# Performance work log

Hardware: AMD Instinct MI355X
Metric: run time of the kernel (lower is better)

The kernel has to match this reference:

```python
import jax, jax.numpy as jnp
import numpy as np

B, N, D_IN, D_HEAD, H, D_EXPAND, D_OUT, D_TIME = 8, 1024, 512, 64, 8, 2048, 512, 256
DQ = D_HEAD * H          # 512
DV = D_IN * H            # 4096
D_QKV = 2 * DQ + 2 * DQ + DV
EPS = 1e-5

def _ln(x, g, b):
    m = jnp.mean(x, axis=-1, keepdims=True)
    v = jnp.var(x, axis=-1, keepdims=True)
    return (x - m) * jax.lax.rsqrt(v + EPS) * g + b

def _swish(x):
    return x * jax.nn.sigmoid(x)

def setup_inputs() -> dict:
    key = jax.random.key(0)
    ks = jax.random.split(key, 16)
    def lin(k, fan_in, fan_out):
        lim = 1.0 / np.sqrt(fan_in)
        kw, kb = jax.random.split(k)
        W = jax.random.uniform(kw, (fan_in, fan_out), jnp.float32, -lim, lim)
        b = jax.random.uniform(kb, (fan_out,), jnp.float32, -lim, lim)
        return W, b
    x = jax.random.normal(ks[0], (B, N, D_IN), jnp.float32)
    t = jax.random.normal(ks[1], (B, D_TIME), jnp.float32)
    Wqkv, bqkv = lin(ks[2], D_IN, D_QKV)
    Wm, bm = lin(ks[3], D_IN * H, D_IN)
    Wt1, bt1 = lin(ks[4], D_TIME, D_TIME)
    Wt2, bt2 = lin(ks[5], D_TIME, D_IN)
    Wf1, bf1 = lin(ks[6], D_IN, D_EXPAND)
    Wf2, bf2 = lin(ks[7], D_EXPAND, D_OUT)
    return {
        "x": x, "t": t,
        "ln1_g": jnp.ones((D_IN,)), "ln1_b": jnp.zeros((D_IN,)),
        "Wqkv": Wqkv, "bqkv": bqkv,
        "lam": jnp.float32(0.5),
        "Wm": Wm, "bm": bm,
        "Wt1": Wt1, "bt1": bt1, "Wt2": Wt2, "bt2": bt2,
        "lnf_g": jnp.ones((D_IN,)), "lnf_b": jnp.zeros((D_IN,)),
        "Wf1": Wf1, "bf1": bf1, "Wf2": Wf2, "bf2": bf2,
    }

def reference(x, t, ln1_g, ln1_b, Wqkv, bqkv, lam, Wm, bm,
              Wt1, bt1, Wt2, bt2, lnf_g, lnf_b, Wf1, bf1, Wf2, bf2):
    scale = D_HEAD ** (-0.5)
    qkv = _ln(x, ln1_g, ln1_b) @ Wqkv + bqkv            # [B,N,D_QKV]
    q1, q2, k1, k2, v = jnp.split(qkv, [DQ, 2 * DQ, 3 * DQ, 4 * DQ], axis=-1)
    hsplit = lambda a, c: a.reshape(B, N, H, c)          # [B,N,H,C]
    q1, q2 = hsplit(q1, D_HEAD), hsplit(q2, D_HEAD)
    k1, k2 = hsplit(k1, D_HEAD), hsplit(k2, D_HEAD)
    v = hsplit(v, D_IN)
    s1 = jax.nn.softmax(jnp.einsum('bnhc,bmhc->bhnm', q1, k1) * scale, axis=-1)
    s2 = jax.nn.softmax(jnp.einsum('bnhc,bmhc->bhnm', q2, k2) * scale, axis=-1)
    attn = s1 - lam * s2                                 # differential attention
    out = jnp.einsum('bhnm,bmhc->bnhc', attn, v).reshape(B, N, H * D_IN)
    x2 = x + out @ Wm + bm
    tp = (_swish(t @ Wt1 + bt1) @ Wt2 + bt2)[:, None, :]  # [B,1,d_in]
    h = _ln(x2 + tp, lnf_g, lnf_b)
    ff = _swish(h @ Wf1 + bf1) @ Wf2 + bf2
    return x2 + ff  # shortcut is identity (d_in == d_out)
```

## Files before the change

kernel.cpp:

```cpp
#include <hip/hip_runtime.h>

#define B_    8
#define N_    1024
#define DIN   512
#define H_    8
#define DH    64
#define DQKV  6144
#define DEXP  2048
#define DTIME 256

typedef __attribute__((ext_vector_type(8))) short s16x8;
typedef __attribute__((ext_vector_type(4))) short s16x4;
typedef __attribute__((ext_vector_type(4))) float f32x4;

__device__ __forceinline__ unsigned short f2bf(float f) {
  unsigned int u = __float_as_uint(f);
  u = (u + 0x7fffu + ((u >> 16) & 1u)) >> 16;
  return (unsigned short)u;
}

__device__ __forceinline__ void gload_lds16(const unsigned short* g, unsigned short* l) {
  __builtin_amdgcn_global_load_lds(
      (const __attribute__((address_space(1))) unsigned int*)(g),
      (__attribute__((address_space(3))) unsigned int*)(l), 16, 0, 0);
}

#define WAITV(n) do { asm volatile("s_waitcnt vmcnt(" #n ")" ::: "memory"); \
                      __builtin_amdgcn_sched_barrier(0); } while (0)
#define WAITL0() do { asm volatile("s_waitcnt lgkmcnt(0)" ::: "memory"); \
                      __builtin_amdgcn_sched_barrier(0); } while (0)

__global__ __launch_bounds__(256) void ln_k(
    const float* __restrict__ x, const float* __restrict__ add,
    const float* __restrict__ g, const float* __restrict__ bb,
    unsigned short* __restrict__ out)
{
  int row = blockIdx.x;
  int tid = threadIdx.x;
  const float* xr = x + (size_t)row * DIN;
  float v0 = xr[tid], v1 = xr[tid + 256];
  if (add) {
    const float* ar = add + (size_t)(row >> 10) * DIN;
    v0 += ar[tid]; v1 += ar[tid + 256];
  }
  float s = v0 + v1, sq = v0 * v0 + v1 * v1;
  #pragma unroll
  for (int m = 1; m < 64; m <<= 1) { s += __shfl_xor(s, m, 64); sq += __shfl_xor(sq, m, 64); }
  __shared__ float red[8];
  int w = tid >> 6;
  if ((tid & 63) == 0) { red[w] = s; red[4 + w] = sq; }
  __syncthreads();
  s  = red[0] + red[1] + red[2] + red[3];
  sq = red[4] + red[5] + red[6] + red[7];
  float mean = s * (1.0f / DIN);
  float var  = sq * (1.0f / DIN) - mean * mean;
  float rs = rsqrtf(var + 1e-5f);
  unsigned short* orow = out + (size_t)row * DIN;
  orow[tid]       = f2bf((v0 - mean) * rs * g[tid]       + bb[tid]);
  orow[tid + 256] = f2bf((v1 - mean) * rs * g[tid + 256] + bb[tid + 256]);
}

__global__ __launch_bounds__(256) void wtrans_k(
    const float* __restrict__ in, unsigned short* __restrict__ out, int R, int C)
{
  __shared__ float tile[32][33];
  int tx = threadIdx.x & 31, ty = threadIdx.x >> 5;
  int c0 = blockIdx.x * 32, r0 = blockIdx.y * 32;
  #pragma unroll
  for (int k = 0; k < 4; ++k)
    tile[ty + k * 8][tx] = in[(size_t)(r0 + ty + k * 8) * C + c0 + tx];
  __syncthreads();
  #pragma unroll
  for (int k = 0; k < 4; ++k)
    out[(size_t)(c0 + ty + k * 8) * R + r0 + tx] = f2bf(tile[tx][ty + k * 8]);
}

__global__ __launch_bounds__(256) void time_k(
    const float* __restrict__ t, const float* __restrict__ Wt1, const float* __restrict__ bt1,
    const float* __restrict__ Wt2, const float* __restrict__ bt2, float* __restrict__ tp)
{
  int b = blockIdx.x, tid = threadIdx.x;
  __shared__ float tl[256], hl[256];
  tl[tid] = t[(size_t)b * 256 + tid];
  __syncthreads();
  float a = bt1[tid];
  for (int k = 0; k < 256; ++k) a += tl[k] * Wt1[(size_t)k * 256 + tid];
  hl[tid] = a / (1.0f + __expf(-a));
  __syncthreads();
  for (int j = tid; j < 512; j += 256) {
    float a2 = bt2[j];
    for (int k = 0; k < 256; ++k) a2 += hl[k] * Wt2[(size_t)k * 512 + j];
    tp[(size_t)b * 512 + j] = a2;
  }
}

template<int EPI>
__global__ __launch_bounds__(256) void gemm_bt(
    const unsigned short* __restrict__ A, int lda,
    const unsigned short* __restrict__ Bt,
    const float* __restrict__ bias, const float* __restrict__ res,
    void* __restrict__ C, int ldc, int N, int K,
    unsigned short* __restrict__ vtout)
{
  __shared__ __attribute__((aligned(16))) unsigned short As[2 * 8192];
  __shared__ __attribute__((aligned(16))) unsigned short Bs[2 * 8192];
  int tid = threadIdx.x;
  int m0 = blockIdx.y * 128, n0 = blockIdx.x * 128;
  int lane = tid & 63, wid = tid >> 6;
  int wr = wid >> 1, wc = wid & 1;
  int lr = lane & 15, lg = lane >> 4, lk = lg * 8;
  f32x4 zero = {0.f, 0.f, 0.f, 0.f};
  f32x4 acc[4][4];
  #pragma unroll
  for (int i = 0; i < 4; ++i)
    #pragma unroll
    for (int j = 0; j < 4; ++j) acc[i][j] = zero;
  int srow = wid * 8 + (lane >> 3);
  int scol = ((lane & 7) ^ (lane >> 3)) * 8;
  const unsigned short* gA = A  + (size_t)(m0 + srow) * lda + scol;
  const unsigned short* gB = Bt + (size_t)(n0 + srow) * K + scol;
  int nk = K >> 6;
  #pragma unroll
  for (int i = 0; i < 4; ++i) {
    gload_lds16(gA + (size_t)(i * 32) * lda, As + (i * 32 + wid * 8) * 64);
    gload_lds16(gB + (size_t)(i * 32) * K,   Bs + (i * 32 + wid * 8) * 64);
  }
  __syncthreads();
#define GSWZ(Lb, base, row, colu) \
  (*(const s16x8*)&(Lb)[(base) + (row) * 64 + (((colu) ^ (((row) & 7) * 8)))])
  for (int kq = 0; kq < nk; ++kq) {
    int cur = (kq & 1) * 8192;
    if (kq + 1 < nk) {
      int nxt = ((kq + 1) & 1) * 8192;
      int kt = (kq + 1) * 64;
      #pragma unroll
      for (int i = 0; i < 4; ++i) {
        gload_lds16(gA + (size_t)(i * 32) * lda + kt, As + nxt + (i * 32 + wid * 8) * 64);
        gload_lds16(gB + (size_t)(i * 32) * K   + kt, Bs + nxt + (i * 32 + wid * 8) * 64);
      }
    }
    s16x8 af[4][2], bf[4][2];
    #pragma unroll
    for (int mf = 0; mf < 4; ++mf) {
      int row = wr * 64 + mf * 16 + lr;
      af[mf][0] = GSWZ(As, cur, row, lk);
      af[mf][1] = GSWZ(As, cur, row, 32 + lk);
    }
    #pragma unroll
    for (int nf = 0; nf < 4; ++nf) {
      int row = wc * 64 + nf * 16 + lr;
      bf[nf][0] = GSWZ(Bs, cur, row, lk);
      bf[nf][1] = GSWZ(Bs, cur, row, 32 + lk);
    }
    #pragma unroll
    for (int mf = 0; mf < 4; ++mf)
      #pragma unroll
      for (int nf = 0; nf < 4; ++nf) {
        acc[mf][nf] = __builtin_amdgcn_mfma_f32_16x16x32_bf16(af[mf][0], bf[nf][0], acc[mf][nf], 0, 0, 0);
        acc[mf][nf] = __builtin_amdgcn_mfma_f32_16x16x32_bf16(af[mf][1], bf[nf][1], acc[mf][nf], 0, 0, 0);
      }
    __syncthreads();
  }
#undef GSWZ
  if (EPI == 3 && n0 >= 2048) {
    #pragma unroll
    for (int mf = 0; mf < 4; ++mf) {
      int row = m0 + wr * 64 + mf * 16 + lg * 4;
      int bb = row >> 10, nn = row & 1023;
      #pragma unroll
      for (int nf = 0; nf < 4; ++nf) {
        int col = n0 + wc * 64 + nf * 16 + lr;
        float bcol = bias[col];
        int hc = col - 2048;
        int hh = hc >> 9, cc = hc & 511;
        unsigned short pk[4];
        #pragma unroll
        for (int r = 0; r < 4; ++r) pk[r] = f2bf(acc[mf][nf][r] + bcol);
        *(s16x4*)(vtout + ((size_t)((bb * 8 + hh) * 512 + cc)) * 1024 + nn) = *(const s16x4*)pk;
      }
    }
    return;
  }
  #pragma unroll
  for (int mf = 0; mf < 4; ++mf)
    #pragma unroll
    for (int nf = 0; nf < 4; ++nf) {
      int col = n0 + wc * 64 + nf * 16 + lr;
      float bcol = bias[col];
      #pragma unroll
      for (int r = 0; r < 4; ++r) {
        int row = m0 + wr * 64 + mf * 16 + lg * 4 + r;
        float v = acc[mf][nf][r] + bcol;
        if (EPI == 1) v = v / (1.0f + __expf(-v));
        if (EPI == 2) {
          v += res[(size_t)row * N + col];
          ((float*)C)[(size_t)row * ldc + col] = v;
        } else {
          ((unsigned short*)C)[(size_t)row * ldc + col] = f2bf(v);
        }
      }
    }
}

__global__ __launch_bounds__(512) void attn_k(
    const unsigned short* __restrict__ qkv, const unsigned short* __restrict__ vt,
    const float* __restrict__ lamp, unsigned short* __restrict__ aout )
{
  const float scale = 0.125f;
  __shared__ __attribute__((aligned(16))) unsigned short KP[33792];
  int w0 = blockIdx.x;
  int bx = (w0 & 7) * 64 + (w0 >> 3);
  int bh = bx >> 3, qt = bx & 7;
  int b = bh >> 3, h = bh & 7;
  int tid = threadIdx.x;
  int lane = tid & 63, w = tid >> 6;
  int lr = lane & 15, lg = lane >> 4, lk = lg * 8;
  int qc1 = h * 64, qc2 = 512 + h * 64, kc1 = 1024 + h * 64, kc2 = 1536 + h * 64;
  f32x4 zero = {0.f, 0.f, 0.f, 0.f};
  const unsigned short* kvbase = qkv + (size_t)(b * N_) * DQKV;

  int srw = lane >> 4;
  int ci0 = (lane & 15) ^ srw;
  int ci1 = (lane & 15) ^ (4 + srw);
  int scol0 = (ci0 < 8) ? (kc1 + ci0 * 8) : (kc2 + (ci0 - 8) * 8);
  int scol1 = (ci1 < 8) ? (kc1 + ci1 * 8) : (kc2 + (ci1 - 8) * 8);

  s16x8 q1f[2], q2f[2];
  {
    size_t ro = (size_t)(b * N_ + qt * 128 + w * 16 + lr) * DQKV;
    q1f[0] = *(const s16x8*)(qkv + ro + qc1 + lk);
    q1f[1] = *(const s16x8*)(qkv + ro + qc1 + 32 + lk);
    q2f[0] = *(const s16x8*)(qkv + ro + qc2 + lk);
    q2f[1] = *(const s16x8*)(qkv + ro + qc2 + 32 + lk);
  }

#define STAGE_K(Lb, kt)                                                              \
  do {                                                                               \
    gload_lds16(kvbase + (size_t)((kt) * 64 + w * 8 + srw) * DQKV + scol0,           \
                (Lb) + (w * 8) * 128);                                               \
    gload_lds16(kvbase + (size_t)((kt) * 64 + w * 8 + 4 + srw) * DQKV + scol1,       \
                (Lb) + (w * 8 + 4) * 128);                                           \
  } while (0)

#define KREAD(Lb, row, colu) (*(const s16x8*)&(Lb)[(row) * 128 + ((colu) ^ (((row) & 7) * 8))])

  unsigned short* Kb0 = KP;
  unsigned short* Kb1 = KP + 8192;
  unsigned short* Pb  = KP + 16384;

  float lp1[4] = {0.f, 0.f, 0.f, 0.f}, lp2[4] = {0.f, 0.f, 0.f, 0.f};
  {
    STAGE_K(Kb0, 0);
    __syncthreads();
    for (int kt = 0; kt < 16; ++kt) {
      unsigned short* Lb = (kt & 1) ? Kb1 : Kb0;
      STAGE_K((kt & 1) ? Kb0 : Kb1, (kt + 1) & 15);
      f32x4 s1[4], s2[4];
      #pragma unroll
      for (int nf = 0; nf < 4; ++nf) {
        int row = nf * 16 + lr;
        s16x8 a0 = KREAD(Lb, row, lk);
        s16x8 a1 = KREAD(Lb, row, 32 + lk);
        s16x8 b0 = KREAD(Lb, row, 64 + lk);
        s16x8 b1 = KREAD(Lb, row, 96 + lk);
        f32x4 t1 = __builtin_amdgcn_mfma_f32_16x16x32_bf16(q1f[0], a0, zero, 0, 0, 0);
        s1[nf]   = __builtin_amdgcn_mfma_f32_16x16x32_bf16(q1f[1], a1, t1, 0, 0, 0);
        f32x4 t2 = __builtin_amdgcn_mfma_f32_16x16x32_bf16(q2f[0], b0, zero, 0, 0, 0);
        s2[nf]   = __builtin_amdgcn_mfma_f32_16x16x32_bf16(q2f[1], b1, t2, 0, 0, 0);
      }
      #pragma unroll
      for (int nf = 0; nf < 4; ++nf)
        #pragma unroll
        for (int r = 0; r < 4; ++r) {
          lp1[r] += __expf(s1[nf][r] * scale);
          lp2[r] += __expf(s2[nf][r] * scale);
        }
      __syncthreads();
    }
    #pragma unroll
    for (int r = 0; r < 4; ++r)
      #pragma unroll
      for (int d = 1; d < 16; d <<= 1) {
        lp1[r] += __shfl_xor(lp1[r], d, 64);
        lp2[r] += __shfl_xor(lp2[r], d, 64);
      }
  }
  float lam = *lamp;
  float r1v[4], r2v[4];
  #pragma unroll
  for (int r = 0; r < 4; ++r) { r1v[r] = 1.f / lp1[r]; r2v[r] = lam / lp2[r]; }

  f32x4 O[8][4];
  #pragma unroll
  for (int mf = 0; mf < 8; ++mf)
    #pragma unroll
    for (int nf = 0; nf < 4; ++nf) O[mf][nf] = zero;

  auto qk_to_p = [&](const unsigned short* Lb, unsigned short* Pt) {
    f32x4 s1[4], s2[4];
    #pragma unroll
    for (int nf = 0; nf < 4; ++nf) {
      int row = nf * 16 + lr;
      s16x8 a0 = KREAD(Lb, row, lk);
      s16x8 a1 = KREAD(Lb, row, 32 + lk);
      s16x8 b0 = KREAD(Lb, row, 64 + lk);
      s16x8 b1 = KREAD(Lb, row, 96 + lk);
      f32x4 t1 = __builtin_amdgcn_mfma_f32_16x16x32_bf16(q1f[0], a0, zero, 0, 0, 0);
      s1[nf]   = __builtin_amdgcn_mfma_f32_16x16x32_bf16(q1f[1], a1, t1, 0, 0, 0);
      f32x4 t2 = __builtin_amdgcn_mfma_f32_16x16x32_bf16(q2f[0], b0, zero, 0, 0, 0);
      s2[nf]   = __builtin_amdgcn_mfma_f32_16x16x32_bf16(q2f[1], b1, t2, 0, 0, 0);
    }
    #pragma unroll
    for (int nf = 0; nf < 4; ++nf)
      #pragma unroll
      for (int r = 0; r < 4; ++r) {
        float p = __expf(s1[nf][r] * scale) * r1v[r]
                - __expf(s2[nf][r] * scale) * r2v[r];
        Pt[(w * 16 + lg * 4 + r) * 68 + nf * 16 + lr] = f2bf(p);
      }
  };

  qk_to_p(Kb0, Pb);
  STAGE_K(Kb1, 1);
  WAITV(0);
  WAITL0();
  __builtin_amdgcn_s_barrier();

  for (int kt = 0; kt < 16; ++kt) {
    unsigned short* Pcur = Pb + (kt & 1) * 8704;
    unsigned short* Pnxt = Pb + ((kt + 1) & 1) * 8704;
    unsigned short* Knxt = ((kt + 1) & 1) ? Kb1 : Kb0;
    unsigned short* Kstg = (kt & 1) ? Kb1 : Kb0;
    int staged = 0;
    if (kt + 2 < 16) { STAGE_K(Kstg, kt + 2); staged = 1; }
    s16x8 vf[4][2];
    #pragma unroll
    for (int nf = 0; nf < 4; ++nf)
      #pragma unroll
      for (int kq = 0; kq < 2; ++kq)
        vf[nf][kq] = *(const s16x8*)(vt + (size_t)(bh * 512 + w * 64 + nf * 16 + lr) * N_
                                     + kt * 64 + kq * 32 + lk);
    if (kt + 1 < 16) qk_to_p(Knxt, Pnxt);
    __builtin_amdgcn_s_setprio(1);
    #pragma unroll
    for (int mf = 0; mf < 8; ++mf) {
      s16x8 pf0 = *(const s16x8*)&Pcur[(mf * 16 + lr) * 68 + lk];
      s16x8 pf1 = *(const s16x8*)&Pcur[(mf * 16 + lr) * 68 + 32 + lk];
      #pragma unroll
      for (int nf = 0; nf < 4; ++nf) {
        O[mf][nf] = __builtin_amdgcn_mfma_f32_16x16x32_bf16(pf0, vf[nf][0], O[mf][nf], 0, 0, 0);
        O[mf][nf] = __builtin_amdgcn_mfma_f32_16x16x32_bf16(pf1, vf[nf][1], O[mf][nf], 0, 0, 0);
      }
    }
    __builtin_amdgcn_s_setprio(0);
    if (kt < 15) {
      if (staged) { WAITV(8); }
      else        { WAITV(0); }
      WAITL0();
      __builtin_amdgcn_s_barrier();
    }
  }
#undef STAGE_K
#undef KREAD
  #pragma unroll
  for (int mf = 0; mf < 8; ++mf)
    #pragma unroll
    for (int nf = 0; nf < 4; ++nf) {
      int col = h * 512 + w * 64 + nf * 16 + lr;
      #pragma unroll
      for (int r = 0; r < 4; ++r) {
        int row = b * N_ + qt * 128 + mf * 16 + lg * 4 + r;
        aout[(size_t)row * DQKV + col] = f2bf(O[mf][nf][r]);
      }
    }
}

extern "C" void kernel_launch(void* const* d_in, const int* in_sizes, int n_in,
                              void* d_out, int out_size, void* d_ws, size_t ws_size,
                              hipStream_t stream) {
  const float* x    = (const float*)d_in[0];
  const float* t    = (const float*)d_in[1];
  const float* ln1g = (const float*)d_in[2];
  const float* ln1b = (const float*)d_in[3];
  const float* Wqkv = (const float*)d_in[4];
  const float* bqkv = (const float*)d_in[5];
  const float* lam  = (const float*)d_in[6];
  const float* Wm   = (const float*)d_in[7];
  const float* bm   = (const float*)d_in[8];
  const float* Wt1  = (const float*)d_in[9];
  const float* bt1  = (const float*)d_in[10];
  const float* Wt2  = (const float*)d_in[11];
  const float* bt2  = (const float*)d_in[12];
  const float* lnfg = (const float*)d_in[13];
  const float* lnfb = (const float*)d_in[14];
  const float* Wf1  = (const float*)d_in[15];
  const float* bf1  = (const float*)d_in[16];
  const float* Wf2  = (const float*)d_in[17];
  const float* bf2  = (const float*)d_in[18];
  float* out = (float*)d_out;
  char* ws = (char*)d_ws;

  unsigned short* qkv   = (unsigned short*)(ws);
  unsigned short* vt    = (unsigned short*)(ws + 100663296ull);
  float*          x2    = (float*)(ws + 167772160ull);
  unsigned short* xn    = (unsigned short*)(ws + 184549376ull);
  unsigned short* WqkvT = (unsigned short*)(ws + 193986560ull);
  unsigned short* WmT   = (unsigned short*)(ws + 200278016ull);
  unsigned short* Wf1T  = (unsigned short*)(ws + 204472320ull);
  unsigned short* Wf2T  = (unsigned short*)(ws + 206569472ull);
  float*          tp    = (float*)(ws + 208666624ull);
  unsigned short* ff1s  = qkv;
  unsigned short* aout  = qkv + 2048;

  wtrans_k<<<dim3(DQKV / 32, DIN / 32),  256, 0, stream>>>(Wqkv, WqkvT, DIN, DQKV);
  wtrans_k<<<dim3(DIN / 32, 4096 / 32),  256, 0, stream>>>(Wm,   WmT,   4096, DIN);
  wtrans_k<<<dim3(DEXP / 32, DIN / 32),  256, 0, stream>>>(Wf1,  Wf1T,  DIN, DEXP);
  wtrans_k<<<dim3(DIN / 32, DEXP / 32),  256, 0, stream>>>(Wf2,  Wf2T,  DEXP, DIN);
  ln_k<<<8192, 256, 0, stream>>>(x, nullptr, ln1g, ln1b, xn);
  time_k<<<8, 256, 0, stream>>>(t, Wt1, bt1, Wt2, bt2, tp);
  gemm_bt<3><<<dim3(DQKV / 128, 8192 / 128), 256, 0, stream>>>(
      xn, DIN, WqkvT, bqkv, nullptr, qkv, DQKV, DQKV, DIN, vt);
  attn_k<<<512, 512, 0, stream>>>(qkv, vt, lam, aout);
  gemm_bt<2><<<dim3(DIN / 128, 8192 / 128), 256, 0, stream>>>(
      aout, DQKV, WmT, bm, x, x2, DIN, DIN, 4096, nullptr);
  ln_k<<<8192, 256, 0, stream>>>(x2, tp, lnfg, lnfb, xn);
  gemm_bt<1><<<dim3(DEXP / 128, 8192 / 128), 256, 0, stream>>>(
      xn, DIN, Wf1T, bf1, nullptr, ff1s, DEXP, DEXP, DIN, nullptr);
  gemm_bt<2><<<dim3(DIN / 128, 8192 / 128), 256, 0, stream>>>(
      ff1s, DEXP, Wf2T, bf2, x2, out, DIN, DIN, DEXP, nullptr);
}
```

Before: 481.5 us.

## Enlarge GEMM tile to 256 rows and software-pipeline attention normalizer pass

Templates the bf16 GEMM on its M tile size so the QKV and FF1 projections use 256x128 tiles with 512 threads, sharing each B tile across more rows and halving the grid. The attention kernel's first pass, which sums softmax denominators, is restructured so the next tile's QK MFMAs are issued before the current tile's exp sums. K staging and waits now use explicit vmcnt/lgkmcnt waits with raw barriers instead of __syncthreads. The larger tiles double LDS for A and raise thread count, which may lower occupancy, and the hand-placed waits add sync complexity.

```diff
diff --git a/kernel.cpp b/kernel.cpp
--- a/kernel.cpp
+++ b/kernel.cpp
@@ -94,18 +94,20 @@
   }
 }
 
-template<int EPI>
-__global__ __launch_bounds__(256) void gemm_bt(
+template<int EPI, int BM>
+__global__ __launch_bounds__(BM * 2) void gemm_bt(
     const unsigned short* __restrict__ A, int lda,
     const unsigned short* __restrict__ Bt,
     const float* __restrict__ bias, const float* __restrict__ res,
     void* __restrict__ C, int ldc, int N, int K,
     unsigned short* __restrict__ vtout)
 {
-  __shared__ __attribute__((aligned(16))) unsigned short As[2 * 8192];
+  __shared__ __attribute__((aligned(16))) unsigned short As[2 * BM * 64];
   __shared__ __attribute__((aligned(16))) unsigned short Bs[2 * 8192];
+  constexpr int TR = BM / 4;
+  constexpr int NB = 512 / BM;
   int tid = threadIdx.x;
-  int m0 = blockIdx.y * 128, n0 = blockIdx.x * 128;
+  int m0 = blockIdx.y * BM, n0 = blockIdx.x * 128;
   int lane = tid & 63, wid = tid >> 6;
   int wr = wid >> 1, wc = wid & 1;
   int lr = lane & 15, lg = lane >> 4, lk = lg * 8;
@@ -121,36 +123,40 @@
   const unsigned short* gB = Bt + (size_t)(n0 + srow) * K + scol;
   int nk = K >> 6;
   #pragma unroll
-  for (int i = 0; i < 4; ++i) {
-    gload_lds16(gA + (size_t)(i * 32) * lda, As + (i * 32 + wid * 8) * 64);
-    gload_lds16(gB + (size_t)(i * 32) * K,   Bs + (i * 32 + wid * 8) * 64);
-  }
+  for (int i = 0; i < 4; ++i)
+    gload_lds16(gA + (size_t)(i * TR) * lda, As + (i * TR + wid * 8) * 64);
+  #pragma unroll
+  for (int i = 0; i < NB; ++i)
+    gload_lds16(gB + (size_t)(i * TR) * K, Bs + (i * TR + wid * 8) * 64);
   __syncthreads();
 #define GSWZ(Lb, base, row, colu) \
   (*(const s16x8*)&(Lb)[(base) + (row) * 64 + (((colu) ^ (((row) & 7) * 8)))])
   for (int kq = 0; kq < nk; ++kq) {
-    int cur = (kq & 1) * 8192;
+    int curA = (kq & 1) * (BM * 64);
+    int curB = (kq & 1) * 8192;
     if (kq + 1 < nk) {
-      int nxt = ((kq + 1) & 1) * 8192;
+      int nxtA = ((kq + 1) & 1) * (BM * 64);
+      int nxtB = ((kq + 1) & 1) * 8192;
       int kt = (kq + 1) * 64;
       #pragma unroll
-      for (int i = 0; i < 4; ++i) {
-        gload_lds16(gA + (size_t)(i * 32) * lda + kt, As + nxt + (i * 32 + wid * 8) * 64);
-        gload_lds16(gB + (size_t)(i * 32) * K   + kt, Bs + nxt + (i * 32 + wid * 8) * 64);
-      }
+      for (int i = 0; i < 4; ++i)
+        gload_lds16(gA + (size_t)(i * TR) * lda + kt, As + nxtA + (i * TR + wid * 8) * 64);
+      #pragma unroll
+      for (int i = 0; i < NB; ++i)
+        gload_lds16(gB + (size_t)(i * TR) * K + kt, Bs + nxtB + (i * TR + wid * 8) * 64);
     }
     s16x8 af[4][2], bf[4][2];
     #pragma unroll
     for (int mf = 0; mf < 4; ++mf) {
       int row = wr * 64 + mf * 16 + lr;
-      af[mf][0] = GSWZ(As, cur, row, lk);
-      af[mf][1] = GSWZ(As, cur, row, 32 + lk);
+      af[mf][0] = GSWZ(As, curA, row, lk);
+      af[mf][1] = GSWZ(As, curA, row, 32 + lk);
     }
     #pragma unroll
     for (int nf = 0; nf < 4; ++nf) {
       int row = wc * 64 + nf * 16 + lr;
-      bf[nf][0] = GSWZ(Bs, cur, row, lk);
-      bf[nf][1] = GSWZ(Bs, cur, row, 32 + lk);
+      bf[nf][0] = GSWZ(Bs, curB, row, lk);
+      bf[nf][1] = GSWZ(Bs, curB, row, 32 + lk);
     }
     #pragma unroll
     for (int mf = 0; mf < 4; ++mf)
@@ -248,56 +254,7 @@
   unsigned short* Kb1 = KP + 8192;
   unsigned short* Pb  = KP + 16384;
 
-  float lp1[4] = {0.f, 0.f, 0.f, 0.f}, lp2[4] = {0.f, 0.f, 0.f, 0.f};
-  {
-    STAGE_K(Kb0, 0);
-    __syncthreads();
-    for (int kt = 0; kt < 16; ++kt) {
-      unsigned short* Lb = (kt & 1) ? Kb1 : Kb0;
-      STAGE_K((kt & 1) ? Kb0 : Kb1, (kt + 1) & 15);
-      f32x4 s1[4], s2[4];
-      #pragma unroll
-      for (int nf = 0; nf < 4; ++nf) {
-        int row = nf * 16 + lr;
-        s16x8 a0 = KREAD(Lb, row, lk);
-        s16x8 a1 = KREAD(Lb, row, 32 + lk);
-        s16x8 b0 = KREAD(Lb, row, 64 + lk);
-        s16x8 b1 = KREAD(Lb, row, 96 + lk);
-        f32x4 t1 = __builtin_amdgcn_mfma_f32_16x16x32_bf16(q1f[0], a0, zero, 0, 0, 0);
-        s1[nf]   = __builtin_amdgcn_mfma_f32_16x16x32_bf16(q1f[1], a1, t1, 0, 0, 0);
-        f32x4 t2 = __builtin_amdgcn_mfma_f32_16x16x32_bf16(q2f[0], b0, zero, 0, 0, 0);
-        s2[nf]   = __builtin_amdgcn_mfma_f32_16x16x32_bf16(q2f[1], b1, t2, 0, 0, 0);
-      }
-      #pragma unroll
-      for (int nf = 0; nf < 4; ++nf)
-        #pragma unroll
-        for (int r = 0; r < 4; ++r) {
-          lp1[r] += __expf(s1[nf][r] * scale);
-          lp2[r] += __expf(s2[nf][r] * scale);
-        }
-      __syncthreads();
-    }
-    #pragma unroll
-    for (int r = 0; r < 4; ++r)
-      #pragma unroll
-      for (int d = 1; d < 16; d <<= 1) {
-        lp1[r] += __shfl_xor(lp1[r], d, 64);
-        lp2[r] += __shfl_xor(lp2[r], d, 64);
-      }
-  }
-  float lam = *lamp;
-  float r1v[4], r2v[4];
-  #pragma unroll
-  for (int r = 0; r < 4; ++r) { r1v[r] = 1.f / lp1[r]; r2v[r] = lam / lp2[r]; }
-
-  f32x4 O[8][4];
-  #pragma unroll
-  for (int mf = 0; mf < 8; ++mf)
-    #pragma unroll
-    for (int nf = 0; nf < 4; ++nf) O[mf][nf] = zero;
-
-  auto qk_to_p = [&](const unsigned short* Lb, unsigned short* Pt) {
-    f32x4 s1[4], s2[4];
+  auto qk_tile = [&](const unsigned short* Lb, f32x4 (&s1)[4], f32x4 (&s2)[4]) {
     #pragma unroll
     for (int nf = 0; nf < 4; ++nf) {
       int row = nf * 16 + lr;
@@ -310,6 +267,59 @@
       f32x4 t2 = __builtin_amdgcn_mfma_f32_16x16x32_bf16(q2f[0], b0, zero, 0, 0, 0);
       s2[nf]   = __builtin_amdgcn_mfma_f32_16x16x32_bf16(q2f[1], b1, t2, 0, 0, 0);
     }
+  };
+
+  float lp1[4] = {0.f, 0.f, 0.f, 0.f}, lp2[4] = {0.f, 0.f, 0.f, 0.f};
+  {
+    f32x4 sc1[4], sc2[4], sn1[4], sn2[4];
+    STAGE_K(Kb0, 0);
+    WAITV(0);
+    __builtin_amdgcn_s_barrier();
+    qk_tile(Kb0, sc1, sc2);
+    WAITL0();
+    STAGE_K(Kb1, 1);
+    WAITV(0);
+    __builtin_amdgcn_s_barrier();
+    for (int kt = 0; kt < 16; ++kt) {
+      if (kt < 15) qk_tile((kt + 1) & 1 ? Kb1 : Kb0, sn1, sn2);
+      WAITL0();
+      if (kt < 14) STAGE_K(kt & 1 ? Kb1 : Kb0, kt + 2);
+      #pragma unroll
+      for (int nf = 0; nf < 4; ++nf)
+        #pragma unroll
+        for (int r = 0; r < 4; ++r) {
+          lp1[r] += __expf(sc1[nf][r] * scale);
+          lp2[r] += __expf(sc2[nf][r] * scale);
+        }
+      if (kt < 15) {
+        #pragma unroll
+        for (int nf = 0; nf < 4; ++nf) { sc1[nf] = sn1[nf]; sc2[nf] = sn2[nf]; }
+      }
+      WAITV(0);
+      __builtin_amdgcn_s_barrier();
+    }
+    #pragma unroll
+    for (int r = 0; r < 4; ++r)
+      #pragma unroll
+      for (int d = 1; d < 16; d <<= 1) {
+        lp1[r] += __shfl_xor(lp1[r], d, 64);
+        lp2[r] += __shfl_xor(lp2[r], d, 64);
+      }
+  }
+  float lam = *lamp;
+  float r1v[4], r2v[4];
+  #pragma unroll
+  for (int r = 0; r < 4; ++r) { r1v[r] = 1.f / lp1[r]; r2v[r] = lam / lp2[r]; }
+
+  f32x4 O[8][4];
+  #pragma unroll
+  for (int mf = 0; mf < 8; ++mf)
+    #pragma unroll
+    for (int nf = 0; nf < 4; ++nf) O[mf][nf] = zero;
+
+  auto qk_to_p = [&](const unsigned short* Lb, unsigned short* Pt) {
+    f32x4 s1[4], s2[4];
+    qk_tile(Lb, s1, s2);
     #pragma unroll
     for (int nf = 0; nf < 4; ++nf)
       #pragma unroll
@@ -320,6 +330,9 @@
       }
   };
 
+  STAGE_K(Kb0, 0);
+  WAITV(0);
+  __builtin_amdgcn_s_barrier();
   qk_to_p(Kb0, Pb);
   STAGE_K(Kb1, 1);
   WAITV(0);
@@ -418,14 +431,14 @@
   wtrans_k<<<dim3(DIN / 32, DEXP / 32),  256, 0, stream>>>(Wf2,  Wf2T,  DEXP, DIN);
   ln_k<<<8192, 256, 0, stream>>>(x, nullptr, ln1g, ln1b, xn);
   time_k<<<8, 256, 0, stream>>>(t, Wt1, bt1, Wt2, bt2, tp);
-  gemm_bt<3><<<dim3(DQKV / 128, 8192 / 128), 256, 0, stream>>>(
+  gemm_bt<3, 256><<<dim3(DQKV / 128, 8192 / 256), 512, 0, stream>>>(
       xn, DIN, WqkvT, bqkv, nullptr, qkv, DQKV, DQKV, DIN, vt);
   attn_k<<<512, 512, 0, stream>>>(qkv, vt, lam, aout);
-  gemm_bt<2><<<dim3(DIN / 128, 8192 / 128), 256, 0, stream>>>(
+  gemm_bt<2, 128><<<dim3(DIN / 128, 8192 / 128), 256, 0, stream>>>(
       aout, DQKV, WmT, bm, x, x2, DIN, DIN, 4096, nullptr);
   ln_k<<<8192, 256, 0, stream>>>(x2, tp, lnfg, lnfb, xn);
-  gemm_bt<1><<<dim3(DEXP / 128, 8192 / 128), 256, 0, stream>>>(
+  gemm_bt<1, 256><<<dim3(DEXP / 128, 8192 / 256), 512, 0, stream>>>(
       xn, DIN, Wf1T, bf1, nullptr, ff1s, DEXP, DEXP, DIN, nullptr);
-  gemm_bt<2><<<dim3(DIN / 128, 8192 / 128), 256, 0, stream>>>(
+  gemm_bt<2, 128><<<dim3(DIN / 128, 8192 / 128), 256, 0, stream>>>(
       ff1s, DEXP, Wf2T, bf2, x2, out, DIN, DIN, DEXP, nullptr);
 }
```

After: 508.2 us. 5.6% more time.
